# Performance work log

Measured on AMD Instinct MI355X. Metric: run time of the kernel, lower is better.

## Reference

```python
import jax, jax.numpy as jnp
import numpy as np

EPS = 1e-5

def conv1x1(x, w, b):
    # x: [B,C,H,W], w: [O,C], b: [O]
    return jnp.einsum('bchw,oc->bohw', x, w) + b[None, :, None, None]

def bn(x, gamma, beta, mean, var):
    scale = gamma * jax.lax.rsqrt(var + EPS)
    return x * scale[None, :, None, None] + (beta - mean * scale)[None, :, None, None]

def setup_inputs() -> dict:
    key = jax.random.key(0)
    ks = jax.random.split(key, 20)
    B, C, H, W = 4, 64, 512, 512
    O = C
    d = {'feature': jax.random.normal(ks[0], (B, C, H, W), dtype=jnp.float32)}
    i = 1
    for name in ('q', 'k', 'v'):
        d[f'w_{name}'] = jax.random.normal(ks[i], (O, C), dtype=jnp.float32) * 0.05; i += 1
        d[f'b_{name}'] = jnp.zeros((O,), dtype=jnp.float32)
        d[f'gamma_{name}'] = jnp.ones((O,), dtype=jnp.float32)
        d[f'beta_{name}'] = jnp.zeros((O,), dtype=jnp.float32)
        d[f'mean_{name}'] = jax.random.normal(ks[i], (O,), dtype=jnp.float32) * 0.1; i += 1
        d[f'var_{name}'] = jax.random.uniform(ks[i], (O,), dtype=jnp.float32) + 0.5; i += 1
    d['w_out'] = jax.random.normal(ks[i], (O, O), dtype=jnp.float32) * 0.05; i += 1
    d['b_out'] = jnp.zeros((O,), dtype=jnp.float32)
    d['gamma_out'] = jnp.ones((O,), dtype=jnp.float32)
    d['beta_out'] = jnp.zeros((O,), dtype=jnp.float32)
    d['mean_out'] = jax.random.normal(ks[i], (O,), dtype=jnp.float32) * 0.1; i += 1
    d['var_out'] = jax.random.uniform(ks[i], (O,), dtype=jnp.float32) + 0.5
    return d

def reference(feature,
              w_q, b_q, gamma_q, beta_q, mean_q, var_q,
              w_k, b_k, gamma_k, beta_k, mean_k, var_k,
              w_v, b_v, gamma_v, beta_v, mean_v, var_v,
              w_out, b_out, gamma_out, beta_out, mean_out, var_out):
    # feature: [B,C,H,W]; attention treats H as sequence, W as feature dim per (b,c)
    q = bn(conv1x1(feature, w_q, b_q), gamma_q, beta_q, mean_q, var_q)
    k = bn(conv1x1(feature, w_k, b_k), gamma_k, beta_k, mean_k, var_k)
    v = bn(conv1x1(feature, w_v, b_v), gamma_v, beta_v, mean_v, var_v)
    W = q.shape[-1]
    scale = 1.0 / jnp.sqrt(jnp.float32(W))
    # scores: [B,C,H,H] = q @ k^T over the W axis
    scores = jnp.einsum('bchw,bcgw->bchg', q, k) * scale
    attn = jax.nn.softmax(scores, axis=-1)
    attn_out = jnp.einsum('bchg,bcgw->bchw', attn, v)  # [B,C,H,W]
    out = bn(conv1x1(attn_out, w_out, b_out), gamma_out, beta_out, mean_out, var_out)
    # dropout is identity in eval mode
    return out + feature
```

## Files before the change

kernel.cpp:

```cpp
#include <hip/hip_runtime.h>
#include <math.h>

typedef unsigned short u16;
typedef unsigned int u32;
typedef unsigned long long u64;
typedef __attribute__((ext_vector_type(8))) short bf16x8;
typedef __attribute__((ext_vector_type(4))) float f32x4;

#define MFMA16(a,b,c) __builtin_amdgcn_mfma_f32_16x16x32_bf16(a,b,c,0,0,0)

typedef __attribute__((address_space(1))) const unsigned int as1_u32;
typedef __attribute__((address_space(3))) unsigned int as3_u32;
__device__ __forceinline__ void gld16(const u16* g, u16* l){
  __builtin_amdgcn_global_load_lds((as1_u32*)g, (as3_u32*)l, 16, 0, 0);
}

__device__ __forceinline__ u16 f2bf(float x){
  union { float f; u32 u; } v; v.f = x;
  u32 u = v.u;
  return (u16)((u + 0x7fffu + ((u>>16)&1u)) >> 16);
}

__device__ __forceinline__ void memfence(){ asm volatile("" ::: "memory"); }

union B8 { bf16x8 v; u32 u[4]; uint4 q; };

__global__ void k0_prep(const float* wm, const float* bias, const float* gamma,
                        const float* beta, const float* mean, const float* var,
                        float extra, u16* wdst, float* ddst)
{
  int t = threadIdx.x;
  if (t < 64){
    float a0 = gamma[t] * rsqrtf(var[t] + 1e-5f);
    ddst[t] = (beta[t] + (bias[t] - mean[t]) * a0) * extra;
  }
  for (int i = t; i < 4096; i += 256){
    int o = i >> 6;
    float a0 = gamma[o] * rsqrtf(var[o] + 1e-5f);
    wdst[i] = f2bf(wm[i] * a0 * extra);
  }
}

__global__ __launch_bounds__(256,2)
void k1_qkv(const float* __restrict__ f, const u16* __restrict__ wz,
            const float* __restrict__ dz, u16* __restrict__ q,
            u16* __restrict__ kk_, u16* __restrict__ vt)
{
  int bid = blockIdx.x;
  int b  = bid >> 7;
  int ht = (bid >> 3) & 15;
  int wt = bid & 7;
  int tid = threadIdx.x;
  int wv = tid >> 6, lane = tid & 63;
  int l15 = lane & 15, l4 = lane >> 4;
  int h0 = ht * 32;
  int w0 = wt * 64 + wv * 16;

  bf16x8 wa[3][4][2];
  #pragma unroll
  for (int mt=0; mt<3; mt++)
    #pragma unroll
    for (int m=0;m<4;m++)
      #pragma unroll
      for (int ks=0;ks<2;ks++){
        B8 t; t.q = *(const uint4*)(wz + mt*4096 + (m*16+l15)*64 + ks*32 + l4*8);
        wa[mt][m][ks] = t.v;
      }
  f32x4 dv[3][4];
  #pragma unroll
  for (int mt=0;mt<3;mt++)
    #pragma unroll
    for (int m=0;m<4;m++)
      dv[mt][m] = *(const f32x4*)(dz + mt*64 + m*16 + l4*4);

  __shared__ u16 vstage[4][8704];
  u16* vs = vstage[wv];

  B8 bf[2];
  #pragma unroll
  for (int ks=0;ks<2;ks++)
    #pragma unroll
    for (int jj=0;jj<4;jj++){
      int c0 = ks*32 + l4*8 + jj*2;
      size_t i0 = ((size_t)(b*64 + c0)*512 + h0)*512 + w0 + l15;
      bf[ks].u[jj] = (u32)f2bf(f[i0]) | ((u32)f2bf(f[i0 + 262144]) << 16);
    }

  for (int hh=0; hh<32; hh++){
    int h = h0 + hh;
    B8 bfn[2];
    if (hh < 31){
      #pragma unroll
      for (int ks=0;ks<2;ks++)
        #pragma unroll
        for (int jj=0;jj<4;jj++){
          int c0 = ks*32 + l4*8 + jj*2;
          size_t i0 = ((size_t)(b*64 + c0)*512 + h + 1)*512 + w0 + l15;
          bfn[ks].u[jj] = (u32)f2bf(f[i0]) | ((u32)f2bf(f[i0 + 262144]) << 16);
        }
    }
    #pragma unroll
    for (int mt=0; mt<3; mt++){
      f32x4 acc[4];
      #pragma unroll
      for (int m=0;m<4;m++) acc[m] = (f32x4){0.f,0.f,0.f,0.f};
      #pragma unroll
      for (int m=0;m<4;m++)
        #pragma unroll
        for (int ks=0;ks<2;ks++)
          acc[m] = MFMA16(wa[mt][m][ks], bf[ks].v, acc[m]);
      #pragma unroll
      for (int m=0;m<4;m++)
        #pragma unroll
        for (int r=0;r<4;r++){
          float val = acc[m][r] + dv[mt][m][r];
          u16 bv = f2bf(val);
          int o = m*16 + l4*4 + r;
          if (mt==0)      q  [((size_t)(b*64+o)*512 + h)*512 + w0 + l15] = bv;
          else if (mt==1) kk_[((size_t)(b*64+o)*512 + h)*512 + w0 + l15] = bv;
          else            vs[o*136 + l15*8 + (hh&7)] = bv;
        }
    }
    bf[0] = bfn[0]; bf[1] = bfn[1];
    if ((hh&7)==7){
      __syncthreads();
      int hbg = (h - 7) >> 3;
      #pragma unroll
      for (int rr=0; rr<16; rr++){
        int o = rr*4 + l4;
        uint4 d = *(const uint4*)(vs + o*136 + l15*8);
        *(uint4*)(vt + (size_t)(b*64+o)*262144 + (size_t)hbg*4096
                     + (size_t)(w0+l15)*8) = d;
      }
      __syncthreads();
    }
  }
}

__global__ __launch_bounds__(512,2)
void k23_attn(const u16* __restrict__ q, const u16* __restrict__ kten,
              const u16* __restrict__ vt, u16* __restrict__ o2)
{
  int phys = blockIdx.x;
  int x = phys & 7, j = phys >> 3;
  int qt = j & 3, hh = j >> 2;
  int head = x*32 + hh;
  int q0 = qt*128;
  int b = head >> 6, c = head & 63;

  int tid = threadIdx.x;
  int wv = tid >> 6, lane = tid & 63;
  int l15 = lane & 15, l4 = lane >> 4;

  const u16* qh = q    + (size_t)head*262144;
  const u16* kh = kten + (size_t)head*262144;
  const u16* vh = vt   + (size_t)head*262144;

  __shared__ u16 KB[2][16640];
  __shared__ u16 VB[2][16384];
  __shared__ u16 Pt[5120];

  auto stageK = [&](int jt, int buf){
    const u16* src = kh + (size_t)jt*16384;
    #pragma unroll
    for (int i=0;i<4;i++){
      int row = i*8 + wv;
      gld16(src + (size_t)row*512 + lane*8, &KB[buf][row*520 + lane*8]);
    }
  };
  auto stageV = [&](int jt, int buf){
    const u16* src = vh + (size_t)jt*16384;
    #pragma unroll
    for (int i=0;i<4;i++){
      int slot = i*512 + tid;
      int w = slot >> 2, cc = slot & 3;
      int hbl = (cc - (w>>1)) & 3;
      gld16(src + hbl*4096 + w*8, &VB[buf][slot*8]);
    }
  };

  uint4 qreg[16];
  {
    const u16* qrow = qh + (size_t)(q0 + wv*16 + l15)*512;
    #pragma unroll
    for (int ks=0;ks<16;ks++) qreg[ks] = *(const uint4*)(qrow + ks*32 + l4*8);
  }
  stageK(0, 0); stageV(0, 0); stageK(1, 1);
  asm volatile("s_waitcnt vmcnt(4)" ::: "memory");
  __builtin_amdgcn_s_barrier(); memfence();

  f32x4 oacc[32];
  #pragma unroll
  for (int n=0;n<32;n++) oacc[n] = (f32x4){0.f,0.f,0.f,0.f};
  float m_run[4] = {-1e30f,-1e30f,-1e30f,-1e30f};
  float l_run[4] = {0.f,0.f,0.f,0.f};

  const int kbase = l15*520 + l4*8;
  const int vbase = l15*32  + (((l4 + (l15>>1)) & 3) << 3);
  const int pbase = (wv*16 + l15)*40;
  const int prow  = (wv*16 + l4*4)*40;

  for (int jt=0; jt<16; ++jt){
    int cur = jt & 1;
    const u16* Kc = &KB[cur][0];
    const u16* Vc = &VB[cur][0];

    if (jt < 15) stageV(jt+1, cur^1);

    f32x4 sA[2], sB[2];
    #pragma unroll
    for (int n=0;n<2;n++){ sA[n]=(f32x4){0,0,0,0}; sB[n]=(f32x4){0,0,0,0}; }
    __builtin_amdgcn_s_setprio(1);
    #pragma unroll
    for (int ks=0; ks<8; ++ks){
      B8 a; a.q = qreg[ks];
      #pragma unroll
      for (int n=0;n<2;n++){
        B8 bb; bb.q = *(const uint4*)(Kc + kbase + n*8320 + ks*32);
        sA[n] = MFMA16(a.v, bb.v, sA[n]);
      }
    }
    #pragma unroll
    for (int ks=8; ks<16; ++ks){
      B8 a; a.q = qreg[ks];
      #pragma unroll
      for (int n=0;n<2;n++){
        B8 bb; bb.q = *(const uint4*)(Kc + kbase + n*8320 + ks*32);
        sB[n] = MFMA16(a.v, bb.v, sB[n]);
      }
    }
    __builtin_amdgcn_s_setprio(0);
    f32x4 sacc0 = sA[0] + sB[0];
    f32x4 sacc1 = sA[1] + sB[1];

    float pm[4], fc[4];
    bool need = false;
    #pragma unroll
    for (int r=0;r<4;r++){
      float p = fmaxf(sacc0[r], sacc1[r]);
      #pragma unroll
      for (int d=1; d<16; d<<=1) p = fmaxf(p, __shfl_xor(p, d, 64));
      pm[r] = p;
      need = need || (p > m_run[r] + 4.0f);
    }
    if (__any(need ? 1 : 0)){
      #pragma unroll
      for (int r=0;r<4;r++){
        float mn = fmaxf(m_run[r], pm[r]);
        fc[r] = exp2f(m_run[r] - mn);
        m_run[r] = mn;
      }
      #pragma unroll
      for (int n=0;n<32;n++)
        #pragma unroll
        for (int r=0;r<4;r++) oacc[n][r] *= fc[r];
    } else {
      fc[0]=fc[1]=fc[2]=fc[3]=1.0f;
    }
    #pragma unroll
    for (int r=0;r<4;r++){
      float e0 = exp2f(sacc0[r] - m_run[r]);
      float e1 = exp2f(sacc1[r] - m_run[r]);
      float s = e0 + e1;
      #pragma unroll
      for (int d=1; d<16; d<<=1) s += __shfl_xor(s, d, 64);
      l_run[r] = l_run[r]*fc[r] + s;
      Pt[prow + r*40 + l15]      = f2bf(e0);
      Pt[prow + r*40 + 16 + l15] = f2bf(e1);
    }

    asm volatile("s_waitcnt lgkmcnt(0)" ::: "memory");
    __builtin_amdgcn_s_barrier(); memfence();

    if (jt < 14) stageK(jt+2, cur);

    B8 pa; pa.q = *(const uint4*)(Pt + pbase + l4*8);
    __builtin_amdgcn_s_setprio(1);
    #pragma unroll
    for (int n=0;n<32;n++){
      B8 bb; bb.q = *(const uint4*)(Vc + vbase + n*512);
      oacc[n] = MFMA16(pa.v, bb.v, oacc[n]);
    }
    __builtin_amdgcn_s_setprio(0);

    if (jt < 15){
      asm volatile("s_waitcnt lgkmcnt(0)" ::: "memory");
      if (jt < 14) { asm volatile("s_waitcnt vmcnt(4)" ::: "memory"); }
      else         { asm volatile("s_waitcnt vmcnt(0)" ::: "memory"); }
      __builtin_amdgcn_s_barrier(); memfence();
    }
  }

  u16* dst = o2 + (size_t)b*33554432 + 16777216
                + (size_t)(c>>1)*524288 + (c&1);
  #pragma unroll
  for (int r=0;r<4;r++){
    float inv = 1.0f / l_run[r];
    int qq = q0 + wv*16 + l4*4 + r;
    #pragma unroll
    for (int n=0;n<32;n++){
      int w = n*16 + l15;
      dst[(size_t)qq*1024 + w*2] = f2bf(oacc[n][r]*inv);
    }
  }
}

__global__ __launch_bounds__(512,2)
void k4_out(const u16* __restrict__ o2, const u16* __restrict__ wz,
            const float* __restrict__ dz, const float* __restrict__ f,
            float* __restrict__ out)
{
  int bid = blockIdx.x;
  int b = bid >> 9;
  int h = bid & 511;
  int tid = threadIdx.x, wv = tid>>6, lane = tid&63;
  int l15 = lane&15, l4 = lane>>4;

  __shared__ u16 Ost[32*1032];

  const u16* src0 = o2 + (size_t)b*33554432 + 16777216 + (size_t)h*1024;
  #pragma unroll
  for (int jj=0;jj<4;jj++){
    int row = jj*8 + wv;
    const u16* srow = src0 + (size_t)row*524288;
    #pragma unroll
    for (int hf=0;hf<2;hf++){
      gld16(srow + hf*512 + lane*8, &Ost[row*1032 + hf*512 + lane*8]);
    }
  }

  bf16x8 wa[4][2];
  #pragma unroll
  for (int m=0;m<4;m++)
    #pragma unroll
    for (int ks=0;ks<2;ks++){
      B8 t; t.q = *(const uint4*)(wz + 3*4096 + (m*16+l15)*64 + ks*32 + l4*8);
      wa[m][ks] = t.v;
    }
  f32x4 dvv[4];
  #pragma unroll
  for (int m=0;m<4;m++) dvv[m] = *(const f32x4*)(dz + 3*64 + m*16 + l4*4);

  asm volatile("s_waitcnt vmcnt(0)" ::: "memory");
  __syncthreads();

  f32x4 acc[4][4];
  #pragma unroll
  for (int m=0;m<4;m++)
    #pragma unroll
    for (int n=0;n<4;n++) acc[m][n] = (f32x4){0.f,0.f,0.f,0.f};

  const u16* obase = Ost + l4*4128 + wv*128 + l15*2;
  #pragma unroll
  for (int ks=0;ks<2;ks++){
    #pragma unroll
    for (int n=0;n<4;n++){
      B8 bb;
      #pragma unroll
      for (int jj=0;jj<4;jj++)
        bb.u[jj] = *(const u32*)(obase + ks*16512 + jj*1032 + n*32);
      #pragma unroll
      for (int m=0;m<4;m++)
        acc[m][n] = MFMA16(wa[m][ks], bb.v, acc[m][n]);
    }
  }
  #pragma unroll
  for (int m=0;m<4;m++)
    #pragma unroll
    for (int n=0;n<4;n++)
      #pragma unroll
      for (int r=0;r<4;r++){
        int o = m*16 + l4*4 + r;
        int w = wv*64 + n*16 + l15;
        size_t idx = ((size_t)(b*64+o)*512 + h)*512 + w;
        out[idx] = acc[m][n][r] + dvv[m][r] + f[idx];
      }
}

extern "C" void kernel_launch(void* const* d_in, const int* in_sizes, int n_in,
                              void* d_out, int out_size, void* d_ws, size_t ws_size,
                              hipStream_t stream) {
  const float* feat = (const float*)d_in[0];
  char* ws = (char*)d_ws;
  u16*   wz   = (u16*)ws;
  float* dz   = (float*)(ws + 32768);
  u16* bufQ = (u16*)(ws + 65536);
  u16* bufK = bufQ + 67108864ull;
  u16* bufV = bufK + 67108864ull;
  u16* o2   = (u16*)d_out;

  float extraK = 1.4426950408889634f / sqrtf(512.0f);
  for (int m=0; m<4; m++){
    int base = 1 + m*6;
    float extra = (m==1) ? extraK : 1.0f;
    k0_prep<<<dim3(1), dim3(256), 0, stream>>>(
        (const float*)d_in[base+0], (const float*)d_in[base+1],
        (const float*)d_in[base+2], (const float*)d_in[base+3],
        (const float*)d_in[base+4], (const float*)d_in[base+5],
        extra, wz + m*4096, dz + m*64);
  }
  k1_qkv   <<<dim3(512),  dim3(256), 0, stream>>>(feat, wz, dz, bufQ, bufK, bufV);
  k23_attn <<<dim3(1024), dim3(512), 0, stream>>>(bufQ, bufK, bufV, o2);
  k4_out   <<<dim3(2048), dim3(512), 0, stream>>>(o2, wz, dz, feat, (float*)d_out);
}
```

Baseline: 680.4 us.

## Replace double-buffered K/V LDS tiles with single buffers and interleaved staging

Drops the double-buffered K and V shared-memory tiles and uses one buffer each. The next K tile is loaded while the PV MFMAs run, and the next V tile is loaded after them, with extra barriers to separate the phases. This roughly halves LDS use, which could allow more blocks per CU. In exchange, load latency is less hidden and each iteration gains extra barriers and waits.

```diff
diff --git a/kernel.cpp b/kernel.cpp
--- a/kernel.cpp
+++ b/kernel.cpp
@@ -156,37 +156,37 @@
   const u16* kh = kten + (size_t)head*262144;
   const u16* vh = vt   + (size_t)head*262144;
 
-  __shared__ u16 KB[2][16640];
-  __shared__ u16 VB[2][16384];
+  __shared__ u16 KB[16640];
+  __shared__ u16 VB[16384];
   __shared__ u16 Pt[5120];
 
-  auto stageK = [&](int jt, int buf){
+  auto stageK = [&](int jt){
     const u16* src = kh + (size_t)jt*16384;
     #pragma unroll
     for (int i=0;i<4;i++){
       int row = i*8 + wv;
-      gld16(src + (size_t)row*512 + lane*8, &KB[buf][row*520 + lane*8]);
+      gld16(src + (size_t)row*512 + lane*8, &KB[row*520 + lane*8]);
     }
   };
-  auto stageV = [&](int jt, int buf){
+  auto stageV = [&](int jt){
     const u16* src = vh + (size_t)jt*16384;
     #pragma unroll
     for (int i=0;i<4;i++){
       int slot = i*512 + tid;
       int w = slot >> 2, cc = slot & 3;
       int hbl = (cc - (w>>1)) & 3;
-      gld16(src + hbl*4096 + w*8, &VB[buf][slot*8]);
+      gld16(src + hbl*4096 + w*8, &VB[slot*8]);
     }
   };
 
+  stageK(0); stageV(0);
   uint4 qreg[16];
   {
     const u16* qrow = qh + (size_t)(q0 + wv*16 + l15)*512;
     #pragma unroll
     for (int ks=0;ks<16;ks++) qreg[ks] = *(const uint4*)(qrow + ks*32 + l4*8);
   }
-  stageK(0, 0); stageV(0, 0); stageK(1, 1);
-  asm volatile("s_waitcnt vmcnt(4)" ::: "memory");
+  asm volatile("s_waitcnt vmcnt(0)" ::: "memory");
   __builtin_amdgcn_s_barrier(); memfence();
 
   f32x4 oacc[32];
@@ -201,12 +201,6 @@
   const int prow  = (wv*16 + l4*4)*40;
 
   for (int jt=0; jt<16; ++jt){
-    int cur = jt & 1;
-    const u16* Kc = &KB[cur][0];
-    const u16* Vc = &VB[cur][0];
-
-    if (jt < 15) stageV(jt+1, cur^1);
-
     f32x4 sA[2], sB[2];
     #pragma unroll
     for (int n=0;n<2;n++){ sA[n]=(f32x4){0,0,0,0}; sB[n]=(f32x4){0,0,0,0}; }
@@ -216,7 +210,7 @@
       B8 a; a.q = qreg[ks];
       #pragma unroll
       for (int n=0;n<2;n++){
-        B8 bb; bb.q = *(const uint4*)(Kc + kbase + n*8320 + ks*32);
+        B8 bb; bb.q = *(const uint4*)(KB + kbase + n*8320 + ks*32);
         sA[n] = MFMA16(a.v, bb.v, sA[n]);
       }
     }
@@ -225,7 +219,7 @@
       B8 a; a.q = qreg[ks];
       #pragma unroll
       for (int n=0;n<2;n++){
-        B8 bb; bb.q = *(const uint4*)(Kc + kbase + n*8320 + ks*32);
+        B8 bb; bb.q = *(const uint4*)(KB + kbase + n*8320 + ks*32);
         sB[n] = MFMA16(a.v, bb.v, sB[n]);
       }
     }
@@ -272,21 +266,25 @@
     asm volatile("s_waitcnt lgkmcnt(0)" ::: "memory");
     __builtin_amdgcn_s_barrier(); memfence();
 
-    if (jt < 14) stageK(jt+2, cur);
+    if (jt < 15) stageK(jt+1);
+    if (jt < 15) { asm volatile("s_waitcnt vmcnt(4)" ::: "memory"); }
+    else         { asm volatile("s_waitcnt vmcnt(0)" ::: "memory"); }
+    __builtin_amdgcn_s_barrier(); memfence();
 
     B8 pa; pa.q = *(const uint4*)(Pt + pbase + l4*8);
     __builtin_amdgcn_s_setprio(1);
     #pragma unroll
     for (int n=0;n<32;n++){
-      B8 bb; bb.q = *(const uint4*)(Vc + vbase + n*512);
+      B8 bb; bb.q = *(const uint4*)(VB + vbase + n*512);
       oacc[n] = MFMA16(pa.v, bb.v, oacc[n]);
     }
     __builtin_amdgcn_s_setprio(0);
 
     if (jt < 15){
       asm volatile("s_waitcnt lgkmcnt(0)" ::: "memory");
-      if (jt < 14) { asm volatile("s_waitcnt vmcnt(4)" ::: "memory"); }
-      else         { asm volatile("s_waitcnt vmcnt(0)" ::: "memory"); }
+      __builtin_amdgcn_s_barrier(); memfence();
+      stageV(jt+1);
+      asm volatile("s_waitcnt vmcnt(4)" ::: "memory");
       __builtin_amdgcn_s_barrier(); memfence();
     }
   }
```

New measurement: 660.1 us. 1.03x faster.

## Split PV output across waves by W columns with V held in registers

Applied to the files above, without the earlier changes.

The P·V stage is repartitioned. Each wave now owns 64 output columns for all 128 query rows, where before it owned 16 rows across all 512 columns. V tiles are loaded straight from global memory into registers, which removes the shared-memory V double buffer. Per-row rescale factors and the final normalisers are exchanged through a small shared buffer. Dropping the V buffer cuts LDS traffic and footprint, but each wave now reads P for all rows, the V global loads sit on the critical path with less prefetch distance, and the code adds extra shared-memory handoffs.

```diff
diff --git a/kernel.cpp b/kernel.cpp
--- a/kernel.cpp
+++ b/kernel.cpp
@@ -151,14 +151,15 @@
   int tid = threadIdx.x;
   int wv = tid >> 6, lane = tid & 63;
   int l15 = lane & 15, l4 = lane >> 4;
+  int w0 = wv*64;
 
   const u16* qh = q    + (size_t)head*262144;
   const u16* kh = kten + (size_t)head*262144;
   const u16* vh = vt   + (size_t)head*262144;
 
   __shared__ u16 KB[2][16640];
-  __shared__ u16 VB[2][16384];
   __shared__ u16 Pt[5120];
+  __shared__ __attribute__((aligned(16))) float facb[136];
 
   auto stageK = [&](int jt, int buf){
     const u16* src = kh + (size_t)jt*16384;
@@ -168,15 +169,13 @@
       gld16(src + (size_t)row*512 + lane*8, &KB[buf][row*520 + lane*8]);
     }
   };
-  auto stageV = [&](int jt, int buf){
+
+  uint4 vreg[4];
+  auto loadV = [&](int jt){
     const u16* src = vh + (size_t)jt*16384;
     #pragma unroll
-    for (int i=0;i<4;i++){
-      int slot = i*512 + tid;
-      int w = slot >> 2, cc = slot & 3;
-      int hbl = (cc - (w>>1)) & 3;
-      gld16(src + hbl*4096 + w*8, &VB[buf][slot*8]);
-    }
+    for (int t=0;t<4;t++)
+      vreg[t] = *(const uint4*)(src + l4*4096 + (size_t)(w0 + t*16 + l15)*8);
   };
 
   uint4 qreg[16];
@@ -185,27 +184,28 @@
     #pragma unroll
     for (int ks=0;ks<16;ks++) qreg[ks] = *(const uint4*)(qrow + ks*32 + l4*8);
   }
-  stageK(0, 0); stageV(0, 0); stageK(1, 1);
-  asm volatile("s_waitcnt vmcnt(4)" ::: "memory");
+  loadV(0);
+  stageK(0, 0);
+  asm volatile("s_waitcnt vmcnt(0)" ::: "memory");
   __builtin_amdgcn_s_barrier(); memfence();
 
-  f32x4 oacc[32];
-  #pragma unroll
-  for (int n=0;n<32;n++) oacc[n] = (f32x4){0.f,0.f,0.f,0.f};
+  f32x4 oacc[8][4];
+  #pragma unroll
+  for (int t=0;t<8;t++)
+    #pragma unroll
+    for (int n=0;n<4;n++) oacc[t][n] = (f32x4){0.f,0.f,0.f,0.f};
   float m_run[4] = {-1e30f,-1e30f,-1e30f,-1e30f};
   float l_run[4] = {0.f,0.f,0.f,0.f};
 
   const int kbase = l15*520 + l4*8;
-  const int vbase = l15*32  + (((l4 + (l15>>1)) & 3) << 3);
-  const int pbase = (wv*16 + l15)*40;
   const int prow  = (wv*16 + l4*4)*40;
+  const int pabase = l15*40 + l4*8;
 
   for (int jt=0; jt<16; ++jt){
     int cur = jt & 1;
     const u16* Kc = &KB[cur][0];
-    const u16* Vc = &VB[cur][0];
-
-    if (jt < 15) stageV(jt+1, cur^1);
+
+    if (jt < 15) stageK(jt+1, cur^1);
 
     f32x4 sA[2], sB[2];
     #pragma unroll
@@ -243,17 +243,14 @@
       pm[r] = p;
       need = need || (p > m_run[r] + 4.0f);
     }
-    if (__any(need ? 1 : 0)){
+    bool rescaled = (__any(need ? 1 : 0) != 0);
+    if (rescaled){
       #pragma unroll
       for (int r=0;r<4;r++){
         float mn = fmaxf(m_run[r], pm[r]);
         fc[r] = exp2f(m_run[r] - mn);
         m_run[r] = mn;
       }
-      #pragma unroll
-      for (int n=0;n<32;n++)
-        #pragma unroll
-        for (int r=0;r<4;r++) oacc[n][r] *= fc[r];
     } else {
       fc[0]=fc[1]=fc[2]=fc[3]=1.0f;
     }
@@ -268,39 +265,65 @@
       Pt[prow + r*40 + l15]      = f2bf(e0);
       Pt[prow + r*40 + 16 + l15] = f2bf(e1);
     }
+    if (lane == 0) facb[128 + wv] = rescaled ? 1.0f : 0.0f;
+    if (l15 == 0){
+      #pragma unroll
+      for (int r=0;r<4;r++) facb[wv*16 + l4*4 + r] = fc[r];
+    }
 
     asm volatile("s_waitcnt lgkmcnt(0)" ::: "memory");
     __builtin_amdgcn_s_barrier(); memfence();
 
-    if (jt < 14) stageK(jt+2, cur);
-
-    B8 pa; pa.q = *(const uint4*)(Pt + pbase + l4*8);
+    f32x4 fl0 = *(const f32x4*)(facb + 128);
+    f32x4 fl1 = *(const f32x4*)(facb + 132);
+    float flg = fl0[0]+fl0[1]+fl0[2]+fl0[3]+fl1[0]+fl1[1]+fl1[2]+fl1[3];
+    if (flg != 0.0f){
+      #pragma unroll
+      for (int t=0;t<8;t++){
+        f32x4 fcv = *(const f32x4*)(facb + t*16 + l4*4);
+        #pragma unroll
+        for (int n=0;n<4;n++)
+          #pragma unroll
+          for (int r=0;r<4;r++) oacc[t][n][r] *= fcv[r];
+      }
+    }
     __builtin_amdgcn_s_setprio(1);
     #pragma unroll
-    for (int n=0;n<32;n++){
-      B8 bb; bb.q = *(const uint4*)(Vc + vbase + n*512);
-      oacc[n] = MFMA16(pa.v, bb.v, oacc[n]);
+    for (int t=0;t<8;t++){
+      B8 pa; pa.q = *(const uint4*)(Pt + pabase + t*640);
+      #pragma unroll
+      for (int n=0;n<4;n++){
+        B8 bb; bb.q = vreg[n];
+        oacc[t][n] = MFMA16(pa.v, bb.v, oacc[t][n]);
+      }
     }
     __builtin_amdgcn_s_setprio(0);
 
-    if (jt < 15){
-      asm volatile("s_waitcnt lgkmcnt(0)" ::: "memory");
-      if (jt < 14) { asm volatile("s_waitcnt vmcnt(4)" ::: "memory"); }
-      else         { asm volatile("s_waitcnt vmcnt(0)" ::: "memory"); }
-      __builtin_amdgcn_s_barrier(); memfence();
-    }
-  }
-
+    if (jt < 15) loadV(jt+1);
+
+    asm volatile("s_waitcnt lgkmcnt(0)" ::: "memory");
+    if (jt < 15) { asm volatile("s_waitcnt vmcnt(4)" ::: "memory"); }
+    __builtin_amdgcn_s_barrier(); memfence();
+  }
+
+  if (l15 == 0){
+    #pragma unroll
+    for (int r=0;r<4;r++) facb[wv*16 + l4*4 + r] = 1.0f / l_run[r];
+  }
+  __syncthreads();
   u16* dst = o2 + (size_t)b*33554432 + 16777216
                 + (size_t)(c>>1)*524288 + (c&1);
   #pragma unroll
-  for (int r=0;r<4;r++){
-    float inv = 1.0f / l_run[r];
-    int qq = q0 + wv*16 + l4*4 + r;
-    #pragma unroll
-    for (int n=0;n<32;n++){
-      int w = n*16 + l15;
-      dst[(size_t)qq*1024 + w*2] = f2bf(oacc[n][r]*inv);
+  for (int t=0;t<8;t++){
+    f32x4 inv = *(const f32x4*)(facb + t*16 + l4*4);
+    #pragma unroll
+    for (int r=0;r<4;r++){
+      int qq = q0 + t*16 + l4*4 + r;
+      #pragma unroll
+      for (int n=0;n<4;n++){
+        int w = w0 + n*16 + l15;
+        dst[(size_t)qq*1024 + w*2] = f2bf(oacc[t][n][r]*inv[r]);
+      }
     }
   }
 }
```

Result: slower. 731.0 us (+7.4%).
